# Performance work log

Measured on AMD Instinct MI355X. Metric: run time of the kernel, lower is better.

The kernel has to match this reference:

```python
import jax, jax.numpy as jnp
import numpy as np

N, D_IN, D_OUT, RANK, TOPK = 16384, 4096, 4096, 64, 8


def setup_inputs() -> dict:
    key = jax.random.key(0)
    k0, k1, k2, k3, k4 = jax.random.split(key, 5)
    hidden_states = jax.random.normal(k0, (N, D_IN), dtype=jnp.float32)
    # nn.Linear(in, rank): weight [rank, in]; nn.Linear(rank, out): weight [out, rank].
    # Original inits up to zeros; we use random weights so the math path is non-trivial.
    down_w = jax.random.normal(k1, (RANK, D_IN), dtype=jnp.float32) * (1.0 / RANK)
    up_w = jax.random.normal(k2, (D_OUT, RANK), dtype=jnp.float32) * 0.02
    top_k_values = jax.random.uniform(k3, (N, TOPK), dtype=jnp.float32)
    # distinct indices per row (like torch.topk output), values in [0, RANK)
    scores = jax.random.uniform(k4, (N, RANK))
    _, top_k_indices = jax.lax.top_k(scores, TOPK)
    top_k_indices = top_k_indices.astype(jnp.int64)
    return {
        "hidden_states": hidden_states,
        "down_w": down_w,
        "up_w": up_w,
        "top_k_values": top_k_values,
        "top_k_indices": top_k_indices,
    }


def reference(hidden_states, down_w, up_w, top_k_values, top_k_indices):
    # down projection: [N, in] x [rank, in]^T -> [N, rank]
    down = jnp.einsum("ni,ri->nr", hidden_states, down_w)
    # gather top-k slots per row, scale, scatter into zeroed [N, rank]
    gathered = jnp.take_along_axis(down, top_k_indices, axis=1)  # [N, k]
    scaled = gathered * top_k_values
    rows = jnp.arange(down.shape[0])[:, None]
    result = jnp.zeros_like(down).at[rows, top_k_indices].set(scaled)
    # up projection: [N, rank] x [out, rank]^T -> [N, out]
    return jnp.einsum("nr,or->no", result, up_w)
```

## Files before the change

kernel.cpp:

```cpp
#include <hip/hip_runtime.h>
#include <hip/hip_bf16.h>
#include <stdint.h>

#define NROWS 16384
#define D_IN  4096
#define D_OUT 4096
#define RANK  64
#define TOPK  8

typedef __hip_bfloat16 bf16;

__device__ int g_is_fp32;
__device__ int g_idx64;
__device__ float g_up_t[RANK * D_OUT];

__device__ __forceinline__ void unpack8(uint4 raw, float f[8]) {
    const unsigned u0 = raw.x, u1 = raw.y, u2 = raw.z, u3 = raw.w;
    f[0] = __uint_as_float(u0 << 16);
    f[1] = __uint_as_float(u0 & 0xffff0000u);
    f[2] = __uint_as_float(u1 << 16);
    f[3] = __uint_as_float(u1 & 0xffff0000u);
    f[4] = __uint_as_float(u2 << 16);
    f[5] = __uint_as_float(u2 & 0xffff0000u);
    f[6] = __uint_as_float(u3 << 16);
    f[7] = __uint_as_float(u3 & 0xffff0000u);
}

__global__ void probe_dtypes(const unsigned short* __restrict__ hid_u16,
                             const int* __restrict__ idx_i32) {
    if (threadIdx.x != 0 || blockIdx.x != 0) return;
    int plausible = 0;
    for (int i = 0; i < 64; i += 2) {
        int e = (hid_u16[i] >> 7) & 0xff;
        if (e >= 0x70 && e <= 0x8a) plausible++;
    }
    g_is_fp32 = (plausible < 16) ? 1 : 0;
    int oddnz = 0;
    for (int i = 1; i < 64; i += 2)
        if (idx_i32[i] != 0) oddnz++;
    g_idx64 = (oddnz == 0) ? 1 : 0;
}

__global__ __launch_bounds__(256) void transpose_up(const void* __restrict__ up_w) {
    const int m = blockIdx.x * 256 + threadIdx.x;
    const int r = m >> 12;
    const int o = m & (D_OUT - 1);
    float v;
    if (g_is_fp32) v = ((const float*)up_w)[o * RANK + r];
    else           v = __bfloat162float(((const bf16*)up_w)[o * RANK + r]);
    g_up_t[m] = v;
}

__global__ __launch_bounds__(256) void moe_lora_fused(
    const void* __restrict__ hidden,
    const void* __restrict__ down_w,
    const void* __restrict__ topk_vals,
    const void* __restrict__ topk_idx,
    void* __restrict__ out)
{
    const int n = blockIdx.x;
    const int t = threadIdx.x;
    const bool fp32 = (g_is_fp32 != 0);
    const bool idx64 = (g_idx64 != 0);

    __shared__ float red[4][TOPK];
    __shared__ float s_s[TOPK];

    int idx[TOPK];
#pragma unroll
    for (int k = 0; k < TOPK; ++k) {
        int m = n * TOPK + k;
        int v = idx64 ? ((const int*)topk_idx)[2 * m] : ((const int*)topk_idx)[m];
        idx[k] = v & (RANK - 1);
    }

    float acc[TOPK];
#pragma unroll
    for (int k = 0; k < TOPK; ++k) acc[k] = 0.0f;

    if (fp32) {
        const float* hrow = (const float*)hidden + (size_t)n * D_IN;
        const float* dw = (const float*)down_w;
#pragma unroll
        for (int i = 0; i < D_IN / (256 * 4); ++i) {
            const int off = i * 1024 + t * 4;
            const float4 h = *reinterpret_cast<const float4*>(hrow + off);
#pragma unroll
            for (int k = 0; k < TOPK; ++k) {
                const float4 w = *reinterpret_cast<const float4*>(dw + (size_t)idx[k] * D_IN + off);
                acc[k] = fmaf(h.x, w.x, acc[k]);
                acc[k] = fmaf(h.y, w.y, acc[k]);
                acc[k] = fmaf(h.z, w.z, acc[k]);
                acc[k] = fmaf(h.w, w.w, acc[k]);
            }
        }
    } else {
        const bf16* hrow = (const bf16*)hidden + (size_t)n * D_IN;
        const bf16* dw = (const bf16*)down_w;
#pragma unroll
        for (int i = 0; i < D_IN / (256 * 8); ++i) {
            const int off = i * 2048 + t * 8;
            float h[8];
            unpack8(*reinterpret_cast<const uint4*>(hrow + off), h);
#pragma unroll
            for (int k = 0; k < TOPK; ++k) {
                float w[8];
                unpack8(*reinterpret_cast<const uint4*>(dw + (size_t)idx[k] * D_IN + off), w);
#pragma unroll
                for (int j = 0; j < 8; ++j) acc[k] = fmaf(h[j], w[j], acc[k]);
            }
        }
    }

#pragma unroll
    for (int k = 0; k < TOPK; ++k) {
        float v = acc[k];
        for (int s = 32; s > 0; s >>= 1) v += __shfl_down(v, s, 64);
        acc[k] = v;
    }
    const int wave = t >> 6;
    const int lane = t & 63;
    if (lane == 0) {
#pragma unroll
        for (int k = 0; k < TOPK; ++k) red[wave][k] = acc[k];
    }
    __syncthreads();
    if (t < TOPK) {
        float v = red[0][t] + red[1][t] + red[2][t] + red[3][t];
        float scale = fp32 ? ((const float*)topk_vals)[n * TOPK + t]
                           : __bfloat162float(((const bf16*)topk_vals)[n * TOPK + t]);
        s_s[t] = v * scale;
    }
    __syncthreads();

    float s[TOPK];
#pragma unroll
    for (int k = 0; k < TOPK; ++k) s[k] = s_s[k];

    if (fp32) {
        float* orow = (float*)out + (size_t)n * D_OUT;
#pragma unroll
        for (int i = 0; i < D_OUT / (256 * 4); ++i) {
            const int o = i * 1024 + t * 4;
            float4 accO = make_float4(0.f, 0.f, 0.f, 0.f);
#pragma unroll
            for (int k = 0; k < TOPK; ++k) {
                const float4 u = *reinterpret_cast<const float4*>(g_up_t + (size_t)idx[k] * D_OUT + o);
                const float sk = s[k];
                accO.x = fmaf(sk, u.x, accO.x);
                accO.y = fmaf(sk, u.y, accO.y);
                accO.z = fmaf(sk, u.z, accO.z);
                accO.w = fmaf(sk, u.w, accO.w);
            }
            *reinterpret_cast<float4*>(orow + o) = accO;
        }
    } else {
        bf16* orow = (bf16*)out + (size_t)n * D_OUT;
#pragma unroll
        for (int i = 0; i < D_OUT / (256 * 8); ++i) {
            const int o = i * 2048 + t * 8;
            float accO[8];
#pragma unroll
            for (int j = 0; j < 8; ++j) accO[j] = 0.0f;
#pragma unroll
            for (int k = 0; k < TOPK; ++k) {
                const float4 u0 = *reinterpret_cast<const float4*>(g_up_t + (size_t)idx[k] * D_OUT + o);
                const float4 u1 = *reinterpret_cast<const float4*>(g_up_t + (size_t)idx[k] * D_OUT + o + 4);
                const float sk = s[k];
                accO[0] = fmaf(sk, u0.x, accO[0]);
                accO[1] = fmaf(sk, u0.y, accO[1]);
                accO[2] = fmaf(sk, u0.z, accO[2]);
                accO[3] = fmaf(sk, u0.w, accO[3]);
                accO[4] = fmaf(sk, u1.x, accO[4]);
                accO[5] = fmaf(sk, u1.y, accO[5]);
                accO[6] = fmaf(sk, u1.z, accO[6]);
                accO[7] = fmaf(sk, u1.w, accO[7]);
            }
            union { uint4 v; bf16 h[8]; } ou;
#pragma unroll
            for (int j = 0; j < 8; ++j) ou.h[j] = __float2bfloat16(accO[j]);
            *reinterpret_cast<uint4*>(orow + o) = ou.v;
        }
    }
}

extern "C" void kernel_launch(void* const* d_in, const int* in_sizes, int n_in,
                              void* d_out, int out_size, void* d_ws, size_t ws_size,
                              hipStream_t stream) {
    const void* hidden = d_in[0];
    const void* down_w = d_in[1];
    const void* up_w   = d_in[2];
    const void* vals   = d_in[3];
    const void* idx    = d_in[4];

    probe_dtypes<<<1, 64, 0, stream>>>((const unsigned short*)hidden, (const int*)idx);
    transpose_up<<<(RANK * D_OUT) / 256, 256, 0, stream>>>(up_w);
    moe_lora_fused<<<NROWS, 256, 0, stream>>>(hidden, down_w, vals, idx, d_out);
}
```

Measured before the change: 566.4 us.

## Split into per-row score kernel and tiled up-projection with LDS-resident up weights

Replaces the single fused per-row kernel with two kernels. The first computes the scaled top-k scores, using one wave per row instead of a 256-thread block. The second tiles the output into 128-row by 256-column blocks, each loading a slice of up_w into padded shared memory so every thread computes one output column across many rows. This drops the separate transpose kernel and the global transposed copy of up_w, and gives up_w reuse through LDS. The cost is an extra launch, a round trip through the workspace for the scores, and column-wise output stores of one element per thread per row.

```diff
diff --git a/kernel.cpp b/kernel.cpp
--- a/kernel.cpp
+++ b/kernel.cpp
@@ -8,11 +8,14 @@
 #define RANK  64
 #define TOPK  8
 
+#define BCOLS 256
+#define BROWS 128
+#define LSTRIDE 65
+
 typedef __hip_bfloat16 bf16;
 
 __device__ int g_is_fp32;
 __device__ int g_idx64;
-__device__ float g_up_t[RANK * D_OUT];
 
 __device__ __forceinline__ void unpack8(uint4 raw, float f[8]) {
     const unsigned u0 = raw.x, u1 = raw.y, u2 = raw.z, u3 = raw.w;
@@ -41,36 +44,24 @@
     g_idx64 = (oddnz == 0) ? 1 : 0;
 }
 
-__global__ __launch_bounds__(256) void transpose_up(const void* __restrict__ up_w) {
-    const int m = blockIdx.x * 256 + threadIdx.x;
-    const int r = m >> 12;
-    const int o = m & (D_OUT - 1);
-    float v;
-    if (g_is_fp32) v = ((const float*)up_w)[o * RANK + r];
-    else           v = __bfloat162float(((const bf16*)up_w)[o * RANK + r]);
-    g_up_t[m] = v;
-}
-
-__global__ __launch_bounds__(256) void moe_lora_fused(
+__global__ __launch_bounds__(256) void compute_s(
     const void* __restrict__ hidden,
     const void* __restrict__ down_w,
     const void* __restrict__ topk_vals,
     const void* __restrict__ topk_idx,
-    void* __restrict__ out)
+    float* __restrict__ s_out)
 {
-    const int n = blockIdx.x;
-    const int t = threadIdx.x;
+    const int lane = threadIdx.x & 63;
+    const int n = blockIdx.x * 4 + (threadIdx.x >> 6);
     const bool fp32 = (g_is_fp32 != 0);
     const bool idx64 = (g_idx64 != 0);
 
-    __shared__ float red[4][TOPK];
-    __shared__ float s_s[TOPK];
-
     int idx[TOPK];
 #pragma unroll
     for (int k = 0; k < TOPK; ++k) {
-        int m = n * TOPK + k;
-        int v = idx64 ? ((const int*)topk_idx)[2 * m] : ((const int*)topk_idx)[m];
+        const int m = n * TOPK + k;
+        const int v = idx64 ? ((const int*)topk_idx)[2 * m]
+                            : ((const int*)topk_idx)[m];
         idx[k] = v & (RANK - 1);
     }
 
@@ -80,10 +71,10 @@
 
     if (fp32) {
         const float* hrow = (const float*)hidden + (size_t)n * D_IN;
-        const float* dw = (const float*)down_w;
-#pragma unroll
-        for (int i = 0; i < D_IN / (256 * 4); ++i) {
-            const int off = i * 1024 + t * 4;
+        const float* dw   = (const float*)down_w;
+#pragma unroll 2
+        for (int i = 0; i < D_IN / (64 * 4); ++i) {
+            const int off = i * 256 + lane * 4;
             const float4 h = *reinterpret_cast<const float4*>(hrow + off);
 #pragma unroll
             for (int k = 0; k < TOPK; ++k) {
@@ -96,10 +87,10 @@
         }
     } else {
         const bf16* hrow = (const bf16*)hidden + (size_t)n * D_IN;
-        const bf16* dw = (const bf16*)down_w;
-#pragma unroll
-        for (int i = 0; i < D_IN / (256 * 8); ++i) {
-            const int off = i * 2048 + t * 8;
+        const bf16* dw   = (const bf16*)down_w;
+#pragma unroll 2
+        for (int i = 0; i < D_IN / (64 * 8); ++i) {
+            const int off = i * 512 + lane * 8;
             float h[8];
             unpack8(*reinterpret_cast<const uint4*>(hrow + off), h);
 #pragma unroll
@@ -112,74 +103,97 @@
         }
     }
 
+    float mys = 0.0f;
 #pragma unroll
     for (int k = 0; k < TOPK; ++k) {
         float v = acc[k];
-        for (int s = 32; s > 0; s >>= 1) v += __shfl_down(v, s, 64);
-        acc[k] = v;
-    }
-    const int wave = t >> 6;
-    const int lane = t & 63;
-    if (lane == 0) {
-#pragma unroll
-        for (int k = 0; k < TOPK; ++k) red[wave][k] = acc[k];
+#pragma unroll
+        for (int d = 32; d > 0; d >>= 1) v += __shfl_xor(v, d, 64);
+        if (lane == k) mys = v;
+    }
+    if (lane < TOPK) {
+        const int m = n * TOPK + lane;
+        const float scale = fp32 ? ((const float*)topk_vals)[m]
+                                 : __bfloat162float(((const bf16*)topk_vals)[m]);
+        s_out[m] = mys * scale;
+    }
+}
+
+__global__ __launch_bounds__(256) void up_proj(
+    const void* __restrict__ up_w,
+    const float* __restrict__ s_in,
+    const void* __restrict__ topk_idx,
+    void* __restrict__ out)
+{
+    const int t = threadIdx.x;
+    const int c0 = (blockIdx.x & (D_OUT / BCOLS - 1)) * BCOLS;
+    const int n0 = (blockIdx.x / (D_OUT / BCOLS)) * BROWS;
+    const bool fp32 = (g_is_fp32 != 0);
+    const bool idx64 = (g_idx64 != 0);
+
+    __shared__ float s_up[BCOLS * LSTRIDE];
+    __shared__ float s_s[BROWS][TOPK];
+    __shared__ int   s_i[BROWS][TOPK];
+
+    if (fp32) {
+        const float4* src = reinterpret_cast<const float4*>(
+            (const float*)up_w + (size_t)c0 * RANK);
+#pragma unroll
+        for (int j = 0; j < (BCOLS * RANK) / (4 * 256); ++j) {
+            const int m = j * 256 + t;
+            const float4 v = src[m];
+            const int o = m >> 4;
+            const int r = (m & 15) * 4;
+            float* dst = s_up + o * LSTRIDE + r;
+            dst[0] = v.x; dst[1] = v.y; dst[2] = v.z; dst[3] = v.w;
+        }
+    } else {
+        const uint4* src = reinterpret_cast<const uint4*>(
+            (const bf16*)up_w + (size_t)c0 * RANK);
+#pragma unroll
+        for (int j = 0; j < (BCOLS * RANK) / (8 * 256); ++j) {
+            const int m = j * 256 + t;
+            float f[8];
+            unpack8(src[m], f);
+            const int o = m >> 3;
+            const int r = (m & 7) * 8;
+            float* dst = s_up + o * LSTRIDE + r;
+#pragma unroll
+            for (int jj = 0; jj < 8; ++jj) dst[jj] = f[jj];
+        }
+    }
+
+#pragma unroll
+    for (int j = 0; j < (BROWS * TOPK) / 256; ++j) {
+        const int m = j * 256 + t;
+        const int gm = n0 * TOPK + m;
+        const int v = idx64 ? ((const int*)topk_idx)[2 * gm]
+                            : ((const int*)topk_idx)[gm];
+        ((int*)s_i)[m]   = v & (RANK - 1);
+        ((float*)s_s)[m] = s_in[gm];
     }
     __syncthreads();
-    if (t < TOPK) {
-        float v = red[0][t] + red[1][t] + red[2][t] + red[3][t];
-        float scale = fp32 ? ((const float*)topk_vals)[n * TOPK + t]
-                           : __bfloat162float(((const bf16*)topk_vals)[n * TOPK + t]);
-        s_s[t] = v * scale;
-    }
-    __syncthreads();
-
-    float s[TOPK];
-#pragma unroll
-    for (int k = 0; k < TOPK; ++k) s[k] = s_s[k];
-
+
+    const float* myup = s_up + t * LSTRIDE;
     if (fp32) {
-        float* orow = (float*)out + (size_t)n * D_OUT;
-#pragma unroll
-        for (int i = 0; i < D_OUT / (256 * 4); ++i) {
-            const int o = i * 1024 + t * 4;
-            float4 accO = make_float4(0.f, 0.f, 0.f, 0.f);
-#pragma unroll
-            for (int k = 0; k < TOPK; ++k) {
-                const float4 u = *reinterpret_cast<const float4*>(g_up_t + (size_t)idx[k] * D_OUT + o);
-                const float sk = s[k];
-                accO.x = fmaf(sk, u.x, accO.x);
-                accO.y = fmaf(sk, u.y, accO.y);
-                accO.z = fmaf(sk, u.z, accO.z);
-                accO.w = fmaf(sk, u.w, accO.w);
-            }
-            *reinterpret_cast<float4*>(orow + o) = accO;
+        float* orow = (float*)out + (size_t)n0 * D_OUT + c0 + t;
+#pragma unroll 4
+        for (int row = 0; row < BROWS; ++row) {
+            float a = 0.0f;
+#pragma unroll
+            for (int k = 0; k < TOPK; ++k)
+                a = fmaf(s_s[row][k], myup[s_i[row][k]], a);
+            orow[(size_t)row * D_OUT] = a;
         }
     } else {
-        bf16* orow = (bf16*)out + (size_t)n * D_OUT;
-#pragma unroll
-        for (int i = 0; i < D_OUT / (256 * 8); ++i) {
-            const int o = i * 2048 + t * 8;
-            float accO[8];
-#pragma unroll
-            for (int j = 0; j < 8; ++j) accO[j] = 0.0f;
-#pragma unroll
-            for (int k = 0; k < TOPK; ++k) {
-                const float4 u0 = *reinterpret_cast<const float4*>(g_up_t + (size_t)idx[k] * D_OUT + o);
-                const float4 u1 = *reinterpret_cast<const float4*>(g_up_t + (size_t)idx[k] * D_OUT + o + 4);
-                const float sk = s[k];
-                accO[0] = fmaf(sk, u0.x, accO[0]);
-                accO[1] = fmaf(sk, u0.y, accO[1]);
-                accO[2] = fmaf(sk, u0.z, accO[2]);
-                accO[3] = fmaf(sk, u0.w, accO[3]);
-                accO[4] = fmaf(sk, u1.x, accO[4]);
-                accO[5] = fmaf(sk, u1.y, accO[5]);
-                accO[6] = fmaf(sk, u1.z, accO[6]);
-                accO[7] = fmaf(sk, u1.w, accO[7]);
-            }
-            union { uint4 v; bf16 h[8]; } ou;
-#pragma unroll
-            for (int j = 0; j < 8; ++j) ou.h[j] = __float2bfloat16(accO[j]);
-            *reinterpret_cast<uint4*>(orow + o) = ou.v;
+        bf16* orow = (bf16*)out + (size_t)n0 * D_OUT + c0 + t;
+#pragma unroll 4
+        for (int row = 0; row < BROWS; ++row) {
+            float a = 0.0f;
+#pragma unroll
+            for (int k = 0; k < TOPK; ++k)
+                a = fmaf(s_s[row][k], myup[s_i[row][k]], a);
+            orow[(size_t)row * D_OUT] = __float2bfloat16(a);
         }
     }
 }
@@ -192,8 +206,9 @@
     const void* up_w   = d_in[2];
     const void* vals   = d_in[3];
     const void* idx    = d_in[4];
+    float* s_ws = (float*)d_ws;
 
     probe_dtypes<<<1, 64, 0, stream>>>((const unsigned short*)hidden, (const int*)idx);
-    transpose_up<<<(RANK * D_OUT) / 256, 256, 0, stream>>>(up_w);
-    moe_lora_fused<<<NROWS, 256, 0, stream>>>(hidden, down_w, vals, idx, d_out);
-}
+    compute_s<<<NROWS / 4, 256, 0, stream>>>(hidden, down_w, vals, idx, s_ws);
+    up_proj<<<(D_OUT / BCOLS) * (NROWS / BROWS), 256, 0, stream>>>(up_w, s_ws, idx, d_out);
+}
```

After: 588.5 us. +3.9%, slower.

## Assign one wavefront per row and software-prefetch loads in fused LoRA kernel

Applied to the files above, without the earlier changes.

Each 256-thread block now handles four rows, one per 64-lane wavefront, instead of one row per block. This removes the shared-memory reduction and both block barriers; the reduction becomes an xor-shuffle within the wave, and each lane reads its own scales. The fp32 down and up loops are restructured to double-buffer the next slice of hidden, down_w and up_t loads in registers, which raises register pressure (launch bounds now also request 4 blocks). Each wave walks its row serially over 16 iterations, so latency hiding depends on that prefetch and on occupancy.

```diff
diff --git a/kernel.cpp b/kernel.cpp
--- a/kernel.cpp
+++ b/kernel.cpp
@@ -51,27 +51,25 @@
     g_up_t[m] = v;
 }
 
-__global__ __launch_bounds__(256) void moe_lora_fused(
+__global__ __launch_bounds__(256, 4) void moe_fused(
     const void* __restrict__ hidden,
     const void* __restrict__ down_w,
     const void* __restrict__ topk_vals,
     const void* __restrict__ topk_idx,
     void* __restrict__ out)
 {
-    const int n = blockIdx.x;
-    const int t = threadIdx.x;
+    const int lane = threadIdx.x & 63;
+    const int n = blockIdx.x * 4 + (threadIdx.x >> 6);
     const bool fp32 = (g_is_fp32 != 0);
     const bool idx64 = (g_idx64 != 0);
 
-    __shared__ float red[4][TOPK];
-    __shared__ float s_s[TOPK];
-
-    int idx[TOPK];
+    int woff[TOPK];
 #pragma unroll
     for (int k = 0; k < TOPK; ++k) {
-        int m = n * TOPK + k;
-        int v = idx64 ? ((const int*)topk_idx)[2 * m] : ((const int*)topk_idx)[m];
-        idx[k] = v & (RANK - 1);
+        const int m = n * TOPK + k;
+        const int v = idx64 ? ((const int*)topk_idx)[2 * m]
+                            : ((const int*)topk_idx)[m];
+        woff[k] = (v & (RANK - 1)) * D_IN;
     }
 
     float acc[TOPK];
@@ -80,32 +78,50 @@
 
     if (fp32) {
         const float* hrow = (const float*)hidden + (size_t)n * D_IN;
-        const float* dw = (const float*)down_w;
-#pragma unroll
-        for (int i = 0; i < D_IN / (256 * 4); ++i) {
-            const int off = i * 1024 + t * 4;
-            const float4 h = *reinterpret_cast<const float4*>(hrow + off);
-#pragma unroll
-            for (int k = 0; k < TOPK; ++k) {
-                const float4 w = *reinterpret_cast<const float4*>(dw + (size_t)idx[k] * D_IN + off);
-                acc[k] = fmaf(h.x, w.x, acc[k]);
-                acc[k] = fmaf(h.y, w.y, acc[k]);
-                acc[k] = fmaf(h.z, w.z, acc[k]);
-                acc[k] = fmaf(h.w, w.w, acc[k]);
+        const float* dw   = (const float*)down_w;
+        float4 hc, wc[TOPK];
+        {
+            const int off = lane * 4;
+            hc = *reinterpret_cast<const float4*>(hrow + off);
+#pragma unroll
+            for (int k = 0; k < TOPK; ++k)
+                wc[k] = *reinterpret_cast<const float4*>(dw + woff[k] + off);
+        }
+#pragma unroll
+        for (int i = 0; i < 16; ++i) {
+            float4 hn, wn[TOPK];
+            if (i < 15) {
+                const int noff = (i + 1) * 256 + lane * 4;
+                hn = *reinterpret_cast<const float4*>(hrow + noff);
+#pragma unroll
+                for (int k = 0; k < TOPK; ++k)
+                    wn[k] = *reinterpret_cast<const float4*>(dw + woff[k] + noff);
+            }
+#pragma unroll
+            for (int k = 0; k < TOPK; ++k) {
+                acc[k] = fmaf(hc.x, wc[k].x, acc[k]);
+                acc[k] = fmaf(hc.y, wc[k].y, acc[k]);
+                acc[k] = fmaf(hc.z, wc[k].z, acc[k]);
+                acc[k] = fmaf(hc.w, wc[k].w, acc[k]);
+            }
+            if (i < 15) {
+                hc = hn;
+#pragma unroll
+                for (int k = 0; k < TOPK; ++k) wc[k] = wn[k];
             }
         }
     } else {
         const bf16* hrow = (const bf16*)hidden + (size_t)n * D_IN;
-        const bf16* dw = (const bf16*)down_w;
-#pragma unroll
-        for (int i = 0; i < D_IN / (256 * 8); ++i) {
-            const int off = i * 2048 + t * 8;
+        const bf16* dw   = (const bf16*)down_w;
+#pragma unroll
+        for (int i = 0; i < 8; ++i) {
+            const int off = i * 512 + lane * 8;
             float h[8];
             unpack8(*reinterpret_cast<const uint4*>(hrow + off), h);
 #pragma unroll
             for (int k = 0; k < TOPK; ++k) {
                 float w[8];
-                unpack8(*reinterpret_cast<const uint4*>(dw + (size_t)idx[k] * D_IN + off), w);
+                unpack8(*reinterpret_cast<const uint4*>(dw + woff[k] + off), w);
 #pragma unroll
                 for (int j = 0; j < 8; ++j) acc[k] = fmaf(h[j], w[j], acc[k]);
             }
@@ -114,58 +130,64 @@
 
 #pragma unroll
     for (int k = 0; k < TOPK; ++k) {
-        float v = acc[k];
-        for (int s = 32; s > 0; s >>= 1) v += __shfl_down(v, s, 64);
-        acc[k] = v;
-    }
-    const int wave = t >> 6;
-    const int lane = t & 63;
-    if (lane == 0) {
-#pragma unroll
-        for (int k = 0; k < TOPK; ++k) red[wave][k] = acc[k];
-    }
-    __syncthreads();
-    if (t < TOPK) {
-        float v = red[0][t] + red[1][t] + red[2][t] + red[3][t];
-        float scale = fp32 ? ((const float*)topk_vals)[n * TOPK + t]
-                           : __bfloat162float(((const bf16*)topk_vals)[n * TOPK + t]);
-        s_s[t] = v * scale;
-    }
-    __syncthreads();
+#pragma unroll
+        for (int d = 32; d > 0; d >>= 1)
+            acc[k] += __shfl_xor(acc[k], d, 64);
+    }
 
     float s[TOPK];
 #pragma unroll
-    for (int k = 0; k < TOPK; ++k) s[k] = s_s[k];
+    for (int k = 0; k < TOPK; ++k) {
+        const int m = n * TOPK + k;
+        const float scale = fp32 ? ((const float*)topk_vals)[m]
+                                 : __bfloat162float(((const bf16*)topk_vals)[m]);
+        s[k] = acc[k] * scale;
+    }
 
     if (fp32) {
         float* orow = (float*)out + (size_t)n * D_OUT;
-#pragma unroll
-        for (int i = 0; i < D_OUT / (256 * 4); ++i) {
-            const int o = i * 1024 + t * 4;
-            float4 accO = make_float4(0.f, 0.f, 0.f, 0.f);
-#pragma unroll
-            for (int k = 0; k < TOPK; ++k) {
-                const float4 u = *reinterpret_cast<const float4*>(g_up_t + (size_t)idx[k] * D_OUT + o);
-                const float sk = s[k];
-                accO.x = fmaf(sk, u.x, accO.x);
-                accO.y = fmaf(sk, u.y, accO.y);
-                accO.z = fmaf(sk, u.z, accO.z);
-                accO.w = fmaf(sk, u.w, accO.w);
-            }
-            *reinterpret_cast<float4*>(orow + o) = accO;
+        float4 uc[TOPK];
+        {
+            const int off = lane * 4;
+#pragma unroll
+            for (int k = 0; k < TOPK; ++k)
+                uc[k] = *reinterpret_cast<const float4*>(g_up_t + woff[k] + off);
+        }
+#pragma unroll
+        for (int i = 0; i < 16; ++i) {
+            float4 un[TOPK];
+            if (i < 15) {
+                const int noff = (i + 1) * 256 + lane * 4;
+#pragma unroll
+                for (int k = 0; k < TOPK; ++k)
+                    un[k] = *reinterpret_cast<const float4*>(g_up_t + woff[k] + noff);
+            }
+            float4 a = make_float4(0.f, 0.f, 0.f, 0.f);
+#pragma unroll
+            for (int k = 0; k < TOPK; ++k) {
+                a.x = fmaf(s[k], uc[k].x, a.x);
+                a.y = fmaf(s[k], uc[k].y, a.y);
+                a.z = fmaf(s[k], uc[k].z, a.z);
+                a.w = fmaf(s[k], uc[k].w, a.w);
+            }
+            *reinterpret_cast<float4*>(orow + i * 256 + lane * 4) = a;
+            if (i < 15) {
+#pragma unroll
+                for (int k = 0; k < TOPK; ++k) uc[k] = un[k];
+            }
         }
     } else {
         bf16* orow = (bf16*)out + (size_t)n * D_OUT;
 #pragma unroll
-        for (int i = 0; i < D_OUT / (256 * 8); ++i) {
-            const int o = i * 2048 + t * 8;
+        for (int i = 0; i < 8; ++i) {
+            const int o = i * 512 + lane * 8;
             float accO[8];
 #pragma unroll
             for (int j = 0; j < 8; ++j) accO[j] = 0.0f;
 #pragma unroll
             for (int k = 0; k < TOPK; ++k) {
-                const float4 u0 = *reinterpret_cast<const float4*>(g_up_t + (size_t)idx[k] * D_OUT + o);
-                const float4 u1 = *reinterpret_cast<const float4*>(g_up_t + (size_t)idx[k] * D_OUT + o + 4);
+                const float4 u0 = *reinterpret_cast<const float4*>(g_up_t + woff[k] + o);
+                const float4 u1 = *reinterpret_cast<const float4*>(g_up_t + woff[k] + o + 4);
                 const float sk = s[k];
                 accO[0] = fmaf(sk, u0.x, accO[0]);
                 accO[1] = fmaf(sk, u0.y, accO[1]);
@@ -195,5 +217,5 @@
 
     probe_dtypes<<<1, 64, 0, stream>>>((const unsigned short*)hidden, (const int*)idx);
     transpose_up<<<(RANK * D_OUT) / 256, 256, 0, stream>>>(up_w);
-    moe_lora_fused<<<NROWS, 256, 0, stream>>>(hidden, down_w, vals, idx, d_out);
-}
+    moe_fused<<<NROWS / 4, 256, 0, stream>>>(hidden, down_w, vals, idx, d_out);
+}
```

New measurement: 684.3 us. 1.21x slower.
